# Performance work log

Hardware: AMD Instinct MI355X
Metric: run time of the kernel (lower is better)

The kernel has to match this reference:

```python
import jax, jax.numpy as jnp
import numpy as np

N, D, H = 4096, 2048, 16
DK = D // H  # 128


def setup_inputs() -> dict:
    key = jax.random.key(0)
    k0, k1, k2, k3 = jax.random.split(key, 4)
    return {
        "tokens_embedding": jax.random.normal(k0, (N, D), dtype=jnp.float32),
        "w_q": jax.random.normal(k1, (H, D, DK), dtype=jnp.float32),
        "w_k": jax.random.normal(k2, (H, D, DK), dtype=jnp.float32),
        "w_v": jax.random.normal(k3, (H, D, DK), dtype=jnp.float32),
    }


def reference(tokens_embedding, w_q, w_k, w_v):
    # Per-head projections (batched over heads): [H, N, DK]
    q = jnp.einsum('nd,hdk->hnk', tokens_embedding, w_q)
    k = jnp.einsum('nd,hdk->hnk', tokens_embedding, w_k)
    v = jnp.einsum('nd,hdk->hnk', tokens_embedding, w_v)
    # Scaled dot-product attention, softmax over keys (orig dim=1 of [N,N])
    scale = 1.0 / jnp.sqrt(jnp.float32(DK))
    scores = jnp.einsum('hnk,hmk->hnm', q, k) * scale  # [H, N, N]
    attn = jax.nn.softmax(scores, axis=-1)
    out = jnp.einsum('hnm,hmk->hnk', attn, v)  # [H, N, DK]
    # Concat heads along feature dim (head order preserved): [N, H*DK]
    return jnp.transpose(out, (1, 0, 2)).reshape(N, H * DK)
```

## Files before the change

kernel.cpp:

```cpp
#include <hip/hip_runtime.h>
#include <hip/hip_bf16.h>

#define N_TOK 4096
#define D_MODEL 2048
#define NHEAD 16
#define DKH 128

typedef __attribute__((ext_vector_type(8))) short short8v;
typedef __attribute__((ext_vector_type(4))) float f32x4;
typedef __attribute__((ext_vector_type(8))) unsigned short ush8;

static __device__ __forceinline__ unsigned short f2bf(float f) {
  unsigned int x = __float_as_uint(f);
  return (unsigned short)((x + 0x7fffu + ((x >> 16) & 1u)) >> 16);
}
static __device__ __forceinline__ float bf2f(unsigned short u) {
  return __uint_as_float(((unsigned int)u) << 16);
}

static __device__ __forceinline__ void gld16(const void* g, void* l) {
  __builtin_amdgcn_global_load_lds(
      (const __attribute__((address_space(1))) unsigned int*)g,
      (__attribute__((address_space(3))) unsigned int*)l, 16, 0, 0);
}

__global__ __launch_bounds__(256)
void split_e_kernel(const float* __restrict__ E,
                    unsigned short* __restrict__ Eh,
                    unsigned short* __restrict__ El) {
  const size_t i = ((size_t)blockIdx.x * 256 + threadIdx.x) * 8;
  const int n = (int)(i >> 11), d0 = (int)(i & 2047);
  float4 v0 = *reinterpret_cast<const float4*>(E + i);
  float4 v1 = *reinterpret_cast<const float4*>(E + i + 4);
  float f[8] = {v0.x, v0.y, v0.z, v0.w, v1.x, v1.y, v1.z, v1.w};
  ush8 hi, lo;
#pragma unroll
  for (int j = 0; j < 8; ++j) {
    unsigned short hu = f2bf(f[j]);
    hi[j] = hu;
    lo[j] = f2bf(f[j] - bf2f(hu));
  }
  const size_t off = (size_t)n * D_MODEL + (d0 ^ ((n & 7) << 3));
  *reinterpret_cast<ush8*>(Eh + off) = hi;
  *reinterpret_cast<ush8*>(El + off) = lo;
}

__global__ __launch_bounds__(256)
void split_w_kernel(const float* __restrict__ Wq, const float* __restrict__ Wk,
                    const float* __restrict__ Wv,
                    unsigned short* __restrict__ WTh,
                    unsigned short* __restrict__ WTl) {
  __shared__ float tile[64][65];
  const int t = threadIdx.x;
  const int d0 = blockIdx.x * 64;
  const int k0 = blockIdx.y * 64;
  const int mh = blockIdx.z;
  const int mat = mh >> 4, h = mh & 15;
  const float* W = (mat == 0) ? Wq : (mat == 1) ? Wk : Wv;
  const float* Wp = W + (size_t)h * D_MODEL * DKH;
  const float fac = (mat == 0) ? (1.44269504089f / sqrtf(128.0f)) : 1.0f;

  const int rr = t >> 4, c4 = (t & 15) * 4;
#pragma unroll
  for (int p = 0; p < 4; ++p) {
    float4 v = *reinterpret_cast<const float4*>(Wp + (size_t)(d0 + rr + 16 * p) * DKH + k0 + c4);
    tile[rr + 16 * p][c4 + 0] = v.x * fac;
    tile[rr + 16 * p][c4 + 1] = v.y * fac;
    tile[rr + 16 * p][c4 + 2] = v.z * fac;
    tile[rr + 16 * p][c4 + 3] = v.w * fac;
  }
  __syncthreads();
  const int dd0 = (t & 7) * 8, kl = t >> 3;
#pragma unroll
  for (int p = 0; p < 2; ++p) {
    const int kg = k0 + kl + 32 * p;
    ush8 hi, lo;
#pragma unroll
    for (int j = 0; j < 8; ++j) {
      float f = tile[dd0 + j][kl + 32 * p];
      unsigned short hu = f2bf(f);
      hi[j] = hu;
      lo[j] = f2bf(f - bf2f(hu));
    }
    const size_t base = ((size_t)(mat * NHEAD + h) * DKH + kg) * D_MODEL +
                        d0 + (dd0 ^ ((kg & 7) << 3));
    *reinterpret_cast<ush8*>(WTh + base) = hi;
    if (mat < 2) *reinterpret_cast<ush8*>(WTl + base) = lo;
  }
}

template <int MODE>
__global__ __launch_bounds__(256, 2)
void proj_gemm_kernel(const unsigned short* __restrict__ Eh,
                      const unsigned short* __restrict__ El,
                      const unsigned short* __restrict__ WTh,
                      const unsigned short* __restrict__ WTl,
                      unsigned short* __restrict__ Qhi, unsigned short* __restrict__ Qlo,
                      unsigned short* __restrict__ Khi, unsigned short* __restrict__ Klo,
                      unsigned short* __restrict__ Vt, int h0) {
  __shared__ alignas(16) unsigned short Ah[128 * 64];
  __shared__ alignas(16) unsigned short Bh[128 * 64];
  __shared__ alignas(16) unsigned short Al[MODE == 0 ? 128 * 64 : 16];
  __shared__ alignas(16) unsigned short Bl[MODE == 0 ? 128 * 64 : 16];

  const int t = threadIdx.x;
  const int nb = blockIdx.x, hl = blockIdx.y, h = h0 + hl;
  const int mat = (MODE == 0) ? blockIdx.z : 2;
  const int wv = t >> 6, lane = t & 63, fr = lane & 15, fq = lane >> 4;
  const int m0 = (wv >> 1) * 64, n0 = (wv & 1) * 64;

  const char *pAh, *pBh, *pAl = nullptr, *pBl = nullptr;
  if (MODE == 0) {
    pAh = (const char*)(Eh + (size_t)nb * 128 * D_MODEL);
    pAl = (const char*)(El + (size_t)nb * 128 * D_MODEL);
    pBh = (const char*)(WTh + ((size_t)mat * NHEAD + h) * DKH * D_MODEL);
    pBl = (const char*)(WTl + ((size_t)mat * NHEAD + h) * DKH * D_MODEL);
  } else {
    pAh = (const char*)(WTh + ((size_t)2 * NHEAD + h) * DKH * D_MODEL);
    pBh = (const char*)(Eh + (size_t)nb * 128 * D_MODEL);
  }

  f32x4 acc[4][4];
#pragma unroll
  for (int a = 0; a < 4; ++a)
#pragma unroll
    for (int b = 0; b < 4; ++b) acc[a][b] = f32x4{0.f, 0.f, 0.f, 0.f};

  const int srow = t >> 3, sbyte = (t & 7) * 16;

  for (int d0 = 0; d0 < D_MODEL; d0 += 64) {
    __syncthreads();
    {
      const size_t gb = (size_t)d0 * 2 + (size_t)srow * 4096 + sbyte;
#pragma unroll
      for (int j = 0; j < 4; ++j) {
        gld16(pAh + gb + (size_t)j * 32 * 4096, (char*)Ah + j * 4096 + t * 16);
        gld16(pBh + gb + (size_t)j * 32 * 4096, (char*)Bh + j * 4096 + t * 16);
      }
      if (MODE == 0) {
#pragma unroll
        for (int j = 0; j < 4; ++j) {
          gld16(pAl + gb + (size_t)j * 32 * 4096, (char*)Al + j * 4096 + t * 16);
          gld16(pBl + gb + (size_t)j * 32 * 4096, (char*)Bl + j * 4096 + t * 16);
        }
      }
    }
    __syncthreads();
    __builtin_amdgcn_s_setprio(1);
#pragma unroll
    for (int ks = 0; ks < 2; ++ks) {
      short8v ah[4], al[4];
#pragma unroll
      for (int mi = 0; mi < 4; ++mi) {
        const int r = m0 + 16 * mi + fr;
        const int off = (ks * 32 + fq * 8) ^ ((r & 7) << 3);
        ah[mi] = *reinterpret_cast<const short8v*>(&Ah[r * 64 + off]);
        if (MODE == 0) al[mi] = *reinterpret_cast<const short8v*>(&Al[r * 64 + off]);
      }
#pragma unroll
      for (int ni = 0; ni < 4; ++ni) {
        const int rn = n0 + 16 * ni + fr;
        const int offn = (ks * 32 + fq * 8) ^ ((rn & 7) << 3);
        short8v bh = *reinterpret_cast<const short8v*>(&Bh[rn * 64 + offn]);
        if (MODE == 0) {
          short8v bl = *reinterpret_cast<const short8v*>(&Bl[rn * 64 + offn]);
#pragma unroll
          for (int mi = 0; mi < 4; ++mi) {
            acc[mi][ni] = __builtin_amdgcn_mfma_f32_16x16x32_bf16(ah[mi], bh, acc[mi][ni], 0, 0, 0);
            acc[mi][ni] = __builtin_amdgcn_mfma_f32_16x16x32_bf16(ah[mi], bl, acc[mi][ni], 0, 0, 0);
            acc[mi][ni] = __builtin_amdgcn_mfma_f32_16x16x32_bf16(al[mi], bh, acc[mi][ni], 0, 0, 0);
          }
        } else {
#pragma unroll
          for (int mi = 0; mi < 4; ++mi)
            acc[mi][ni] = __builtin_amdgcn_mfma_f32_16x16x32_bf16(ah[mi], bh, acc[mi][ni], 0, 0, 0);
        }
      }
    }
    __builtin_amdgcn_s_setprio(0);
  }

  if (MODE == 0) {
    unsigned short* Ohi = (mat == 0) ? Qhi : Khi;
    unsigned short* Olo = (mat == 0) ? Qlo : Klo;
#pragma unroll
    for (int mi = 0; mi < 4; ++mi)
#pragma unroll
      for (int ni = 0; ni < 4; ++ni)
#pragma unroll
        for (int i = 0; i < 4; ++i) {
          float v = acc[mi][ni][i];
          unsigned short hu = f2bf(v);
          unsigned short lu = f2bf(v - bf2f(hu));
          int n = nb * 128 + m0 + 16 * mi + fq * 4 + i;
          int k = n0 + 16 * ni + fr;
          if (mat == 1) k ^= ((n & 7) << 3);
          size_t off = ((size_t)hl * N_TOK + n) * DKH + k;
          Ohi[off] = hu;
          Olo[off] = lu;
        }
  } else {
#pragma unroll
    for (int mi = 0; mi < 4; ++mi)
#pragma unroll
      for (int ni = 0; ni < 4; ++ni)
#pragma unroll
        for (int i = 0; i < 4; ++i) {
          int kout = m0 + 16 * mi + fq * 4 + i;
          int tn = nb * 128 + n0 + 16 * ni + fr;
          int ts = (tn & ~63) | ((tn & 63) ^ ((kout & 7) << 3));
          Vt[((size_t)hl * DKH + kout) * N_TOK + ts] = f2bf(acc[mi][ni][i]);
        }
  }
}

__global__ __launch_bounds__(256, 2)
void attn_kernel(const unsigned short* __restrict__ Qhi,
                 const unsigned short* __restrict__ Qlo,
                 const unsigned short* __restrict__ Khi,
                 const unsigned short* __restrict__ Klo,
                 const unsigned short* __restrict__ Vt,
                 float* __restrict__ out, int h0, int HC)
{
  __shared__ alignas(16) unsigned short KhiL[64][128];
  __shared__ alignas(16) unsigned short KloL[64][128];
  __shared__ alignas(16) unsigned short VtL[128][64];
  __shared__ alignas(16) unsigned short PL[4][32][64];

  const int t = threadIdx.x;
  int b = blockIdx.x;
  const int nwg = 32 * HC;
  if ((nwg & 7) == 0) b = (b & 7) * (nwg >> 3) + (b >> 3);
  const int qb = b & 31;
  const int hl = b >> 5;
  const int h  = h0 + hl;
  const int wv = t >> 6, lane = t & 63;
  const int fr = lane & 15, fq = lane >> 4;
  const int q0 = qb * 128 + wv * 32;

  short8v qhi[2][4], qlo[2][4];
#pragma unroll
  for (int m = 0; m < 2; ++m) {
    const unsigned short* qp  = Qhi + ((size_t)hl * N_TOK + q0 + m * 16 + fr) * DKH + fq * 8;
    const unsigned short* qp2 = Qlo + ((size_t)hl * N_TOK + q0 + m * 16 + fr) * DKH + fq * 8;
#pragma unroll
    for (int kc = 0; kc < 4; ++kc) {
      qhi[m][kc] = *reinterpret_cast<const short8v*>(qp + kc * 32);
      qlo[m][kc] = *reinterpret_cast<const short8v*>(qp2 + kc * 32);
    }
  }

  f32x4 o[2][8];
#pragma unroll
  for (int m = 0; m < 2; ++m)
#pragma unroll
    for (int i = 0; i < 8; ++i) o[m][i] = f32x4{0.f, 0.f, 0.f, 0.f};
  float mrow[2][4], lrow[2][4];
#pragma unroll
  for (int m = 0; m < 2; ++m)
#pragma unroll
    for (int i = 0; i < 4; ++i) { mrow[m][i] = -__builtin_inff(); lrow[m][i] = 0.f; }

  const char* KhiB = (const char*)(Khi + (size_t)hl * N_TOK * DKH);
  const char* KloB = (const char*)(Klo + (size_t)hl * N_TOK * DKH);
  const char* VtB  = (const char*)(Vt  + (size_t)hl * DKH * N_TOK);
  const int toff = t * 16;
  const int vrow = t >> 3, vbyte = (t & 7) * 16;

  for (int kt = 0; kt < N_TOK / 64; ++kt) {
    const int key0 = kt * 64;
    __syncthreads();
    {
      const char* gk  = KhiB + (size_t)key0 * 256;
      const char* gk2 = KloB + (size_t)key0 * 256;
#pragma unroll
      for (int j = 0; j < 4; ++j)
        gld16(gk + j * 4096 + toff, (char*)&KhiL[0][0] + j * 4096 + toff);
#pragma unroll
      for (int j = 0; j < 4; ++j)
        gld16(gk2 + j * 4096 + toff, (char*)&KloL[0][0] + j * 4096 + toff);
#pragma unroll
      for (int j = 0; j < 4; ++j)
        gld16(VtB + (size_t)(j * 32 + vrow) * (N_TOK * 2) + key0 * 2 + vbyte,
              (char*)&VtL[0][0] + j * 4096 + toff);
    }
    __syncthreads();

    f32x4 s[2][4];
#pragma unroll
    for (int m = 0; m < 2; ++m)
#pragma unroll
      for (int cf = 0; cf < 4; ++cf) s[m][cf] = f32x4{0.f, 0.f, 0.f, 0.f};
    __builtin_amdgcn_s_setprio(1);
#pragma unroll
    for (int cf = 0; cf < 4; ++cf) {
      const int kr = cf * 16 + fr;
      const int csw = ((kr & 7) << 3);
#pragma unroll
      for (int kc = 0; kc < 4; ++kc) {
        short8v bhi = *reinterpret_cast<const short8v*>(&KhiL[kr][(kc * 32 + fq * 8) ^ csw]);
        short8v blo = *reinterpret_cast<const short8v*>(&KloL[kr][(kc * 32 + fq * 8) ^ csw]);
#pragma unroll
        for (int m = 0; m < 2; ++m) {
          s[m][cf] = __builtin_amdgcn_mfma_f32_16x16x32_bf16(qhi[m][kc], bhi, s[m][cf], 0, 0, 0);
          s[m][cf] = __builtin_amdgcn_mfma_f32_16x16x32_bf16(qhi[m][kc], blo, s[m][cf], 0, 0, 0);
          s[m][cf] = __builtin_amdgcn_mfma_f32_16x16x32_bf16(qlo[m][kc], bhi, s[m][cf], 0, 0, 0);
        }
      }
    }
    __builtin_amdgcn_s_setprio(0);

    float mx[2][4];
#pragma unroll
    for (int m = 0; m < 2; ++m)
#pragma unroll
      for (int i = 0; i < 4; ++i) {
        float v = fmaxf(fmaxf(s[m][0][i], s[m][1][i]), fmaxf(s[m][2][i], s[m][3][i]));
        v = fmaxf(v, __shfl_xor(v, 1));
        v = fmaxf(v, __shfl_xor(v, 2));
        v = fmaxf(v, __shfl_xor(v, 4));
        v = fmaxf(v, __shfl_xor(v, 8));
        mx[m][i] = v;
      }
    int upd = 0;
#pragma unroll
    for (int m = 0; m < 2; ++m)
#pragma unroll
      for (int i = 0; i < 4; ++i) upd |= (mx[m][i] > mrow[m][i]);
    if (__any(upd)) {
#pragma unroll
      for (int m = 0; m < 2; ++m)
#pragma unroll
        for (int i = 0; i < 4; ++i) {
          float mn = fmaxf(mrow[m][i], mx[m][i]);
          float al = exp2f(mrow[m][i] - mn);
          mrow[m][i] = mn;
          lrow[m][i] *= al;
#pragma unroll
          for (int of = 0; of < 8; ++of) o[m][of][i] *= al;
        }
    }
    unsigned short pbv[2][4][4];
#pragma unroll
    for (int m = 0; m < 2; ++m)
#pragma unroll
      for (int i = 0; i < 4; ++i) {
        float rs = 0.f;
#pragma unroll
        for (int cf = 0; cf < 4; ++cf) {
          float e = exp2f(s[m][cf][i] - mrow[m][i]);
          unsigned short eb = f2bf(e);
          pbv[m][cf][i] = eb;
          rs += bf2f(eb);
        }
        rs += __shfl_xor(rs, 1); rs += __shfl_xor(rs, 2);
        rs += __shfl_xor(rs, 4); rs += __shfl_xor(rs, 8);
        lrow[m][i] += rs;
      }

#pragma unroll
    for (int m = 0; m < 2; ++m)
#pragma unroll
      for (int cf = 0; cf < 4; ++cf)
#pragma unroll
        for (int i = 0; i < 4; ++i) {
          int prow = fq * 4 + i;
          PL[wv][m * 16 + prow][(cf * 16 + fr) ^ ((prow & 7) << 3)] = pbv[m][cf][i];
        }
    asm volatile("s_waitcnt lgkmcnt(0)" ::: "memory");
    __builtin_amdgcn_sched_barrier(0);

    __builtin_amdgcn_s_setprio(1);
#pragma unroll
    for (int ks = 0; ks < 2; ++ks) {
      short8v pa[2];
#pragma unroll
      for (int m = 0; m < 2; ++m)
        pa[m] = *reinterpret_cast<const short8v*>(
            &PL[wv][m * 16 + fr][(ks * 32 + fq * 8) ^ ((fr & 7) << 3)]);
#pragma unroll
      for (int of = 0; of < 8; ++of) {
        const int dr = of * 16 + fr;
        short8v bv = *reinterpret_cast<const short8v*>(
            &VtL[dr][(ks * 32 + fq * 8) ^ ((dr & 7) << 3)]);
#pragma unroll
        for (int m = 0; m < 2; ++m)
          o[m][of] = __builtin_amdgcn_mfma_f32_16x16x32_bf16(pa[m], bv, o[m][of], 0, 0, 0);
      }
    }
    __builtin_amdgcn_s_setprio(0);
  }

#pragma unroll
  for (int m = 0; m < 2; ++m)
#pragma unroll
    for (int i = 0; i < 4; ++i) {
      float inv = 1.0f / lrow[m][i];
      int n = q0 + m * 16 + fq * 4 + i;
      float* op = out + (size_t)n * (NHEAD * DKH) + h * DKH;
#pragma unroll
      for (int of = 0; of < 8; ++of)
        op[of * 16 + fr] = o[m][of][i] * inv;
    }
}

extern "C" void kernel_launch(void* const* d_in, const int* in_sizes, int n_in,
                              void* d_out, int out_size, void* d_ws, size_t ws_size,
                              hipStream_t stream) {
  (void)in_sizes; (void)n_in; (void)out_size;
  const float* E  = (const float*)d_in[0];
  const float* Wq = (const float*)d_in[1];
  const float* Wk = (const float*)d_in[2];
  const float* Wv = (const float*)d_in[3];
  float* out = (float*)d_out;

  const size_t ND   = (size_t)N_TOK * D_MODEL;
  const size_t WThE = (size_t)3 * NHEAD * DKH * D_MODEL;
  const size_t WTlE = (size_t)2 * NHEAD * DKH * D_MODEL;
  const size_t phe  = (size_t)N_TOK * DKH;
  const size_t baseE = 2 * ND + WThE + WTlE;

  unsigned short* Eh  = (unsigned short*)d_ws;
  unsigned short* El  = Eh + ND;
  unsigned short* WTh = El + ND;
  unsigned short* WTl = WTh + WThE;
  unsigned short* chunk = WTl + WTlE;

  int HC = NHEAD;
  while (HC > 1 && (baseE + (size_t)HC * 5 * phe) * 2 > ws_size) HC >>= 1;

  split_e_kernel<<<dim3((unsigned)(ND / 8 / 256)), 256, 0, stream>>>(E, Eh, El);
  split_w_kernel<<<dim3(32, 2, 48), 256, 0, stream>>>(Wq, Wk, Wv, WTh, WTl);

  for (int h0 = 0; h0 < NHEAD; h0 += HC) {
    unsigned short* Qhi = chunk;
    unsigned short* Qlo = Qhi + (size_t)HC * phe;
    unsigned short* Khi = Qlo + (size_t)HC * phe;
    unsigned short* Klo = Khi + (size_t)HC * phe;
    unsigned short* Vt  = Klo + (size_t)HC * phe;
    proj_gemm_kernel<0><<<dim3(32, HC, 2), 256, 0, stream>>>(Eh, El, WTh, WTl,
                                                             Qhi, Qlo, Khi, Klo, Vt, h0);
    proj_gemm_kernel<1><<<dim3(32, HC, 1), 256, 0, stream>>>(Eh, El, WTh, WTl,
                                                             Qhi, Qlo, Khi, Klo, Vt, h0);
    attn_kernel<<<dim3(32 * HC), 256, 0, stream>>>(Qhi, Qlo, Khi, Klo, Vt, out, h0, HC);
  }
}
```

Before: 568.9 us.

## Compute transposed S^T in attention so each lane owns one query row

The QK^T MFMAs now swap operands, so the score tile comes out transposed and each lane holds scores for a single query column. That cuts per-row max and sum state from 4 values to 1 and shortens each cross-lane reduction to two shuffles. P is packed as 32-bit bf16 pairs into a padded LDS buffer, and the PV MFMA is also transposed so the output can be written as float4 vectors. The extra LDS layout adds some complexity, and the launch order of the two projection kernels is swapped.

```diff
diff --git a/kernel.cpp b/kernel.cpp
--- a/kernel.cpp
+++ b/kernel.cpp
@@ -8,6 +8,7 @@
 
 typedef __attribute__((ext_vector_type(8))) short short8v;
 typedef __attribute__((ext_vector_type(4))) float f32x4;
+typedef __attribute__((ext_vector_type(4))) unsigned short ush4;
 typedef __attribute__((ext_vector_type(8))) unsigned short ush8;
 
 static __device__ __forceinline__ unsigned short f2bf(float f) {
@@ -126,12 +127,10 @@
 #pragma unroll
     for (int b = 0; b < 4; ++b) acc[a][b] = f32x4{0.f, 0.f, 0.f, 0.f};
 
-  const int srow = t >> 3, sbyte = (t & 7) * 16;
-
   for (int d0 = 0; d0 < D_MODEL; d0 += 64) {
     __syncthreads();
     {
-      const size_t gb = (size_t)d0 * 2 + (size_t)srow * 4096 + sbyte;
+      const size_t gb = (size_t)d0 * 2 + (size_t)(t >> 3) * 4096 + (t & 7) * 16;
 #pragma unroll
       for (int j = 0; j < 4; ++j) {
         gld16(pAh + gb + (size_t)j * 32 * 4096, (char*)Ah + j * 4096 + t * 16);
@@ -225,7 +224,7 @@
   __shared__ alignas(16) unsigned short KhiL[64][128];
   __shared__ alignas(16) unsigned short KloL[64][128];
   __shared__ alignas(16) unsigned short VtL[128][64];
-  __shared__ alignas(16) unsigned short PL[4][32][64];
+  __shared__ unsigned int PL32[4][2][32][20];
 
   const int t = threadIdx.x;
   int b = blockIdx.x;
@@ -255,11 +254,8 @@
   for (int m = 0; m < 2; ++m)
 #pragma unroll
     for (int i = 0; i < 8; ++i) o[m][i] = f32x4{0.f, 0.f, 0.f, 0.f};
-  float mrow[2][4], lrow[2][4];
-#pragma unroll
-  for (int m = 0; m < 2; ++m)
-#pragma unroll
-    for (int i = 0; i < 4; ++i) { mrow[m][i] = -__builtin_inff(); lrow[m][i] = 0.f; }
+  float mrow[2] = {-__builtin_inff(), -__builtin_inff()};
+  float lrow[2] = {0.f, 0.f};
 
   const char* KhiB = (const char*)(Khi + (size_t)hl * N_TOK * DKH);
   const char* KloB = (const char*)(Klo + (size_t)hl * N_TOK * DKH);
@@ -286,122 +282,112 @@
     }
     __syncthreads();
 
-    f32x4 s[2][4];
+    f32x4 tt[2][4];
 #pragma unroll
     for (int m = 0; m < 2; ++m)
 #pragma unroll
-      for (int cf = 0; cf < 4; ++cf) s[m][cf] = f32x4{0.f, 0.f, 0.f, 0.f};
+      for (int kf = 0; kf < 4; ++kf) tt[m][kf] = f32x4{0.f, 0.f, 0.f, 0.f};
     __builtin_amdgcn_s_setprio(1);
 #pragma unroll
-    for (int cf = 0; cf < 4; ++cf) {
-      const int kr = cf * 16 + fr;
-      const int csw = ((kr & 7) << 3);
-#pragma unroll
-      for (int kc = 0; kc < 4; ++kc) {
-        short8v bhi = *reinterpret_cast<const short8v*>(&KhiL[kr][(kc * 32 + fq * 8) ^ csw]);
-        short8v blo = *reinterpret_cast<const short8v*>(&KloL[kr][(kc * 32 + fq * 8) ^ csw]);
+    for (int kc = 0; kc < 4; ++kc) {
+      short8v khf[4], klf[4];
+#pragma unroll
+      for (int kf = 0; kf < 4; ++kf) {
+        const int kr = kf * 16 + fr;
+        const int off = (kc * 32 + fq * 8) ^ ((kr & 7) << 3);
+        khf[kf] = *reinterpret_cast<const short8v*>(&KhiL[kr][off]);
+        klf[kf] = *reinterpret_cast<const short8v*>(&KloL[kr][off]);
+      }
+#pragma unroll
+      for (int kf = 0; kf < 4; ++kf)
 #pragma unroll
         for (int m = 0; m < 2; ++m) {
-          s[m][cf] = __builtin_amdgcn_mfma_f32_16x16x32_bf16(qhi[m][kc], bhi, s[m][cf], 0, 0, 0);
-          s[m][cf] = __builtin_amdgcn_mfma_f32_16x16x32_bf16(qhi[m][kc], blo, s[m][cf], 0, 0, 0);
-          s[m][cf] = __builtin_amdgcn_mfma_f32_16x16x32_bf16(qlo[m][kc], bhi, s[m][cf], 0, 0, 0);
-        }
-      }
+          tt[m][kf] = __builtin_amdgcn_mfma_f32_16x16x32_bf16(khf[kf], qhi[m][kc], tt[m][kf], 0, 0, 0);
+          tt[m][kf] = __builtin_amdgcn_mfma_f32_16x16x32_bf16(klf[kf], qhi[m][kc], tt[m][kf], 0, 0, 0);
+          tt[m][kf] = __builtin_amdgcn_mfma_f32_16x16x32_bf16(khf[kf], qlo[m][kc], tt[m][kf], 0, 0, 0);
+        }
     }
     __builtin_amdgcn_s_setprio(0);
 
-    float mx[2][4];
-#pragma unroll
-    for (int m = 0; m < 2; ++m)
-#pragma unroll
-      for (int i = 0; i < 4; ++i) {
-        float v = fmaxf(fmaxf(s[m][0][i], s[m][1][i]), fmaxf(s[m][2][i], s[m][3][i]));
-        v = fmaxf(v, __shfl_xor(v, 1));
-        v = fmaxf(v, __shfl_xor(v, 2));
-        v = fmaxf(v, __shfl_xor(v, 4));
-        v = fmaxf(v, __shfl_xor(v, 8));
-        mx[m][i] = v;
-      }
-    int upd = 0;
-#pragma unroll
-    for (int m = 0; m < 2; ++m)
-#pragma unroll
-      for (int i = 0; i < 4; ++i) upd |= (mx[m][i] > mrow[m][i]);
-    if (__any(upd)) {
-#pragma unroll
-      for (int m = 0; m < 2; ++m)
-#pragma unroll
-        for (int i = 0; i < 4; ++i) {
-          float mn = fmaxf(mrow[m][i], mx[m][i]);
-          float al = exp2f(mrow[m][i] - mn);
-          mrow[m][i] = mn;
-          lrow[m][i] *= al;
-#pragma unroll
-          for (int of = 0; of < 8; ++of) o[m][of][i] *= al;
-        }
-    }
-    unsigned short pbv[2][4][4];
-#pragma unroll
-    for (int m = 0; m < 2; ++m)
-#pragma unroll
-      for (int i = 0; i < 4; ++i) {
-        float rs = 0.f;
-#pragma unroll
-        for (int cf = 0; cf < 4; ++cf) {
-          float e = exp2f(s[m][cf][i] - mrow[m][i]);
-          unsigned short eb = f2bf(e);
-          pbv[m][cf][i] = eb;
-          rs += bf2f(eb);
-        }
-        rs += __shfl_xor(rs, 1); rs += __shfl_xor(rs, 2);
-        rs += __shfl_xor(rs, 4); rs += __shfl_xor(rs, 8);
-        lrow[m][i] += rs;
-      }
-
-#pragma unroll
-    for (int m = 0; m < 2; ++m)
-#pragma unroll
-      for (int cf = 0; cf < 4; ++cf)
-#pragma unroll
-        for (int i = 0; i < 4; ++i) {
-          int prow = fq * 4 + i;
-          PL[wv][m * 16 + prow][(cf * 16 + fr) ^ ((prow & 7) << 3)] = pbv[m][cf][i];
-        }
+    float mx[2];
+#pragma unroll
+    for (int m = 0; m < 2; ++m) {
+      float v = -__builtin_inff();
+#pragma unroll
+      for (int kf = 0; kf < 4; ++kf)
+#pragma unroll
+        for (int i = 0; i < 4; ++i) v = fmaxf(v, tt[m][kf][i]);
+      v = fmaxf(v, __shfl_xor(v, 16));
+      v = fmaxf(v, __shfl_xor(v, 32));
+      mx[m] = v;
+    }
+    if (__any((mx[0] > mrow[0]) | (mx[1] > mrow[1]))) {
+#pragma unroll
+      for (int m = 0; m < 2; ++m) {
+        float mn = fmaxf(mrow[m], mx[m]);
+        float al = exp2f(mrow[m] - mn);
+        mrow[m] = mn;
+        lrow[m] *= al;
+#pragma unroll
+        for (int of = 0; of < 8; ++of)
+#pragma unroll
+          for (int i = 0; i < 4; ++i) o[m][of][i] *= al;
+      }
+    }
+#pragma unroll
+    for (int m = 0; m < 2; ++m) {
+      float rs = 0.f;
+#pragma unroll
+      for (int kf = 0; kf < 4; ++kf)
+#pragma unroll
+        for (int hh = 0; hh < 2; ++hh) {
+          float p0 = exp2f(tt[m][kf][2 * hh]     - mrow[m]);
+          float p1 = exp2f(tt[m][kf][2 * hh + 1] - mrow[m]);
+          unsigned short b0 = f2bf(p0), b1 = f2bf(p1);
+          rs += bf2f(b0) + bf2f(b1);
+          PL32[wv][m][kf * 8 + 2 * fq + hh][fr] = (unsigned)b0 | ((unsigned)b1 << 16);
+        }
+      rs += __shfl_xor(rs, 16);
+      rs += __shfl_xor(rs, 32);
+      lrow[m] += rs;
+    }
     asm volatile("s_waitcnt lgkmcnt(0)" ::: "memory");
     __builtin_amdgcn_sched_barrier(0);
 
     __builtin_amdgcn_s_setprio(1);
 #pragma unroll
     for (int ks = 0; ks < 2; ++ks) {
-      short8v pa[2];
+      union { unsigned u[4]; short8v v; } pb[2];
 #pragma unroll
       for (int m = 0; m < 2; ++m)
-        pa[m] = *reinterpret_cast<const short8v*>(
-            &PL[wv][m * 16 + fr][(ks * 32 + fq * 8) ^ ((fr & 7) << 3)]);
+#pragma unroll
+        for (int w = 0; w < 4; ++w)
+          pb[m].u[w] = PL32[wv][m][16 * ks + 4 * fq + w][fr];
 #pragma unroll
       for (int of = 0; of < 8; ++of) {
         const int dr = of * 16 + fr;
-        short8v bv = *reinterpret_cast<const short8v*>(
+        short8v av = *reinterpret_cast<const short8v*>(
             &VtL[dr][(ks * 32 + fq * 8) ^ ((dr & 7) << 3)]);
 #pragma unroll
         for (int m = 0; m < 2; ++m)
-          o[m][of] = __builtin_amdgcn_mfma_f32_16x16x32_bf16(pa[m], bv, o[m][of], 0, 0, 0);
+          o[m][of] = __builtin_amdgcn_mfma_f32_16x16x32_bf16(av, pb[m].v, o[m][of], 0, 0, 0);
       }
     }
     __builtin_amdgcn_s_setprio(0);
   }
 
 #pragma unroll
-  for (int m = 0; m < 2; ++m)
-#pragma unroll
-    for (int i = 0; i < 4; ++i) {
-      float inv = 1.0f / lrow[m][i];
-      int n = q0 + m * 16 + fq * 4 + i;
-      float* op = out + (size_t)n * (NHEAD * DKH) + h * DKH;
-#pragma unroll
-      for (int of = 0; of < 8; ++of)
-        op[of * 16 + fr] = o[m][of][i] * inv;
-    }
+  for (int m = 0; m < 2; ++m) {
+    float inv = 1.0f / lrow[m];
+    int n = q0 + m * 16 + fr;
+    float* op = out + (size_t)n * (NHEAD * DKH) + h * DKH + fq * 4;
+#pragma unroll
+    for (int of = 0; of < 8; ++of) {
+      float4 r = make_float4(o[m][of][0] * inv, o[m][of][1] * inv,
+                             o[m][of][2] * inv, o[m][of][3] * inv);
+      *reinterpret_cast<float4*>(op + of * 16) = r;
+    }
+  }
 }
 
 extern "C" void kernel_launch(void* const* d_in, const int* in_sizes, int n_in,
@@ -438,10 +424,10 @@
     unsigned short* Khi = Qlo + (size_t)HC * phe;
     unsigned short* Klo = Khi + (size_t)HC * phe;
     unsigned short* Vt  = Klo + (size_t)HC * phe;
+    proj_gemm_kernel<1><<<dim3(32, HC, 1), 256, 0, stream>>>(Eh, El, WTh, WTl,
+                                                             Qhi, Qlo, Khi, Klo, Vt, h0);
     proj_gemm_kernel<0><<<dim3(32, HC, 2), 256, 0, stream>>>(Eh, El, WTh, WTl,
                                                              Qhi, Qlo, Khi, Klo, Vt, h0);
-    proj_gemm_kernel<1><<<dim3(32, HC, 1), 256, 0, stream>>>(Eh, El, WTh, WTl,
-                                                             Qhi, Qlo, Khi, Klo, Vt, h0);
     attn_kernel<<<dim3(32 * HC), 256, 0, stream>>>(Qhi, Qlo, Khi, Klo, Vt, out, h0, HC);
   }
 }
```

Result: faster. 500.3 us (-12.1%).
